# Kernel tuning notes

Hardware: AMD Instinct MI355X
Metric: run time of the kernel (lower is better)

The kernel has to match this reference:

```python
import jax, jax.numpy as jnp
import numpy as np
import math

B = 2048
N_IN, N_H, N_OUT = 1024, 1024, 512
MAX_STEPS = 2                 # number of Gibbs sweeps (original loops until max_steps)
TEMP_A, TEMP_B = 2.0, 5.0     # temp_coeffs: T(step) = A / exp(step / B)
N_UPD = N_H + N_OUT           # visible layer is clamped (x given, unlock_vis=False)


def setup_inputs() -> dict:
    key = jax.random.key(0)
    ks = jax.random.split(key, 9)
    # binary states, as produced by torch.bernoulli(0.5) in init_state
    x = jax.random.bernoulli(ks[0], 0.5, (B, N_IN)).astype(jnp.float32)
    s1_init = jax.random.bernoulli(ks[1], 0.5, (B, N_H)).astype(jnp.float32)
    s2_init = jax.random.bernoulli(ks[2], 0.5, (B, N_OUT)).astype(jnp.float32)
    W1 = jax.random.normal(ks[3], (N_H, N_IN), jnp.float32) * 0.02
    b1 = jax.random.normal(ks[4], (N_H,), jnp.float32) * 0.02
    W2 = jax.random.normal(ks[5], (N_OUT, N_H), jnp.float32) * 0.02
    b2 = jax.random.normal(ks[6], (N_OUT,), jnp.float32) * 0.02
    # one random permutation of the 1536 free units per sweep (torch.randperm)
    ids = jnp.concatenate([
        jax.random.permutation(jax.random.fold_in(ks[7], s), N_UPD)
        for s in range(MAX_STEPS)
    ]).astype(jnp.int32)                      # [MAX_STEPS * N_UPD]
    # uniforms for the Bernoulli draws (torch.rand per node update)
    u = jax.random.uniform(ks[8], (MAX_STEPS * N_UPD, B), jnp.float32)
    return dict(x=x, s1_init=s1_init, s2_init=s2_init,
                W1=W1, b1=b1, W2=W2, b2=b2, u=u, ids=ids)


def reference(x, s1_init, s2_init, W1, b1, W2, b2, u, ids):
    # per-update temperature: sweep s has T = TEMP_A / exp(s / TEMP_B)
    temps = jnp.repeat(
        jnp.array([TEMP_A / math.exp(s / TEMP_B) for s in range(MAX_STEPS)],
                  dtype=jnp.float32),
        N_UPD)                                # [MAX_STEPS * N_UPD]

    def step(carry, inp):
        s1, s2 = carry
        gid, uu, T = inp                      # gid: global unit id in [0, N_UPD)

        def upd_hidden(s1, s2):
            n = gid                           # hidden unit index
            # gap = state[0] @ W1[n,:] + b1[n] + state[2] @ W2[:,n]
            gap = x @ W1[n] + b1[n] + s2 @ W2[:, n]      # [B]
            act = (jax.nn.sigmoid(gap / T) > uu).astype(s1.dtype)
            return s1.at[:, n].set(act), s2

        def upd_output(s1, s2):
            n = gid - N_H                     # output unit index
            # gap = state[1] @ W2[n,:] + b2[n]  (top layer: no layer above)
            gap = s1 @ W2[n] + b2[n]                     # [B]
            act = (jax.nn.sigmoid(gap / T) > uu).astype(s2.dtype)
            return s1, s2.at[:, n].set(act)

        s1, s2 = jax.lax.cond(gid < N_H, upd_hidden, upd_output, s1, s2)
        return (s1, s2), None

    (s1, s2), _ = jax.lax.scan(step, (s1_init, s2_init), (ids, u, temps))
    # state = [x (clamped visible), hidden, output], returned concatenated
    return jnp.concatenate([x, s1, s2], axis=-1)      # [B, N_IN+N_H+N_OUT]
```

## Files before the change

### kernel.cpp

```cpp
#include <hip/hip_runtime.h>
#include <math.h>

#define B_TOT   2048
#define N_IN    1024
#define N_H     1024
#define N_OUT   512
#define N_UPD   1536
#define T_TOT   3072
#define N_WIN   48


__global__ void prep_w1t(const float* __restrict__ W1, float* __restrict__ W1T) {
    int idx = blockIdx.x * 256 + threadIdx.x;
    int r = idx & 1023;
    int c = idx >> 10;
    W1T[(size_t)c * 1024 + r] = W1[(size_t)r * 1024 + c];
}

__global__ void prep_w2tf(const float* __restrict__ W2, float* __restrict__ W2Tf) {
    int idx = blockIdx.x * 256 + threadIdx.x;
    int r = idx & 511;
    int c = idx >> 9;
    W2Tf[(size_t)c * 512 + r] = W2[(size_t)r * 1024 + c];
}

__global__ void prep_whf(const float* __restrict__ W2, float* __restrict__ WHf) {
    int idx = blockIdx.x * 256 + threadIdx.x;
    int n = idx >> 9;
    int r = idx & 511;
    int l = r >> 3, j = r & 7;
    WHf[idx] = W2[(size_t)(j * 64 + l) * 1024 + n];
}

__global__ void prep_wof(const float* __restrict__ W2, float* __restrict__ WOf) {
    int idx = blockIdx.x * 256 + threadIdx.x;
    int nn = idx >> 10;
    int r = idx & 1023;
    int l = r >> 4, j = r & 15;
    WOf[idx] = W2[(size_t)nn * 1024 + j * 64 + l];
}

__global__ void prep_wx(const float* __restrict__ W2, const int* __restrict__ ids,
                        float* __restrict__ WXf) {
    int idx = blockIdx.x * 256 + threadIdx.x;
    int w = idx >> 12;
    int j = (idx >> 6) & 63;
    int l = idx & 63;
    int mj = ids[w * 64 + j];
    int nl = ids[w * 64 + l];
    float v = 0.0f;
    if (mj < N_H && nl >= N_H) v = W2[(size_t)(nl - N_H) * 1024 + mj];
    else if (mj >= N_H && nl < N_H) v = W2[(size_t)(mj - N_H) * 1024 + nl];
    WXf[idx] = v;
}

__global__ void prep_pos(const int* __restrict__ ids, int* __restrict__ posA,
                         int* __restrict__ posB) {
    int t = blockIdx.x * 256 + threadIdx.x;
    int n = ids[t];
    if (t < N_UPD) posA[n] = t; else posB[n] = t - N_UPD;
}

__global__ void prep_pos2(const int* __restrict__ ids, const int* __restrict__ posA,
                          int* __restrict__ pos2) {
    int t = blockIdx.x * 256 + threadIdx.x;
    pos2[t] = posA[ids[N_UPD + t]];
}

__global__ __launch_bounds__(256) void prep_th(const float* __restrict__ u,
                                               double* __restrict__ thT) {
    __shared__ double tile[64][65];
    int bt = blockIdx.x % 48;
    int bb = blockIdx.x / 48;
    int tx = threadIdx.x & 63;
    int ty0 = threadIdx.x >> 6;
    const double T1c = (double)(float)(2.0 / exp((double)1 / 5.0));
    for (int r = ty0; r < 64; r += 4) {
        int t = bt * 64 + r;
        double ud = (double)u[(size_t)t * 2048 + bb * 64 + tx];
        double T = (t >= N_UPD) ? T1c : 2.0;
        tile[r][tx] = T * (log(ud) - log1p(-ud));
    }
    __syncthreads();
    for (int r = ty0; r < 64; r += 4)
        thT[(size_t)(bb * 64 + r) * 3072 + bt * 64 + tx] = tile[tx][r];
}

__global__ void copy_x(const float* __restrict__ x, float* __restrict__ out) {
    int idx = blockIdx.x * 256 + threadIdx.x;
    int b = idx >> 8, c = idx & 255;
    ((float4*)(out + (size_t)b * 2560))[c] = ((const float4*)(x + (size_t)b * 1024))[c];
}


#define FMA32(M, DW) { \
    a0  = fma(((M) & 0x00000001u) ? 1.0 : 0.0, (DW), a0 ); \
    a1  = fma(((M) & 0x00000002u) ? 1.0 : 0.0, (DW), a1 ); \
    a2  = fma(((M) & 0x00000004u) ? 1.0 : 0.0, (DW), a2 ); \
    a3  = fma(((M) & 0x00000008u) ? 1.0 : 0.0, (DW), a3 ); \
    a4  = fma(((M) & 0x00000010u) ? 1.0 : 0.0, (DW), a4 ); \
    a5  = fma(((M) & 0x00000020u) ? 1.0 : 0.0, (DW), a5 ); \
    a6  = fma(((M) & 0x00000040u) ? 1.0 : 0.0, (DW), a6 ); \
    a7  = fma(((M) & 0x00000080u) ? 1.0 : 0.0, (DW), a7 ); \
    a8  = fma(((M) & 0x00000100u) ? 1.0 : 0.0, (DW), a8 ); \
    a9  = fma(((M) & 0x00000200u) ? 1.0 : 0.0, (DW), a9 ); \
    a10 = fma(((M) & 0x00000400u) ? 1.0 : 0.0, (DW), a10); \
    a11 = fma(((M) & 0x00000800u) ? 1.0 : 0.0, (DW), a11); \
    a12 = fma(((M) & 0x00001000u) ? 1.0 : 0.0, (DW), a12); \
    a13 = fma(((M) & 0x00002000u) ? 1.0 : 0.0, (DW), a13); \
    a14 = fma(((M) & 0x00004000u) ? 1.0 : 0.0, (DW), a14); \
    a15 = fma(((M) & 0x00008000u) ? 1.0 : 0.0, (DW), a15); \
    a16 = fma(((M) & 0x00010000u) ? 1.0 : 0.0, (DW), a16); \
    a17 = fma(((M) & 0x00020000u) ? 1.0 : 0.0, (DW), a17); \
    a18 = fma(((M) & 0x00040000u) ? 1.0 : 0.0, (DW), a18); \
    a19 = fma(((M) & 0x00080000u) ? 1.0 : 0.0, (DW), a19); \
    a20 = fma(((M) & 0x00100000u) ? 1.0 : 0.0, (DW), a20); \
    a21 = fma(((M) & 0x00200000u) ? 1.0 : 0.0, (DW), a21); \
    a22 = fma(((M) & 0x00400000u) ? 1.0 : 0.0, (DW), a22); \
    a23 = fma(((M) & 0x00800000u) ? 1.0 : 0.0, (DW), a23); \
    a24 = fma(((M) & 0x01000000u) ? 1.0 : 0.0, (DW), a24); \
    a25 = fma(((M) & 0x02000000u) ? 1.0 : 0.0, (DW), a25); \
    a26 = fma(((M) & 0x04000000u) ? 1.0 : 0.0, (DW), a26); \
    a27 = fma(((M) & 0x08000000u) ? 1.0 : 0.0, (DW), a27); \
    a28 = fma(((M) & 0x10000000u) ? 1.0 : 0.0, (DW), a28); \
    a29 = fma(((M) & 0x20000000u) ? 1.0 : 0.0, (DW), a29); \
    a30 = fma(((M) & 0x40000000u) ? 1.0 : 0.0, (DW), a30); \
    a31 = fma(((M) & 0x80000000u) ? 1.0 : 0.0, (DW), a31); }

#define FMA16(M, DW) { \
    a0  = fma(((M) & 0x0001u) ? 1.0 : 0.0, (DW), a0 ); \
    a1  = fma(((M) & 0x0002u) ? 1.0 : 0.0, (DW), a1 ); \
    a2  = fma(((M) & 0x0004u) ? 1.0 : 0.0, (DW), a2 ); \
    a3  = fma(((M) & 0x0008u) ? 1.0 : 0.0, (DW), a3 ); \
    a4  = fma(((M) & 0x0010u) ? 1.0 : 0.0, (DW), a4 ); \
    a5  = fma(((M) & 0x0020u) ? 1.0 : 0.0, (DW), a5 ); \
    a6  = fma(((M) & 0x0040u) ? 1.0 : 0.0, (DW), a6 ); \
    a7  = fma(((M) & 0x0080u) ? 1.0 : 0.0, (DW), a7 ); \
    a8  = fma(((M) & 0x0100u) ? 1.0 : 0.0, (DW), a8 ); \
    a9  = fma(((M) & 0x0200u) ? 1.0 : 0.0, (DW), a9 ); \
    a10 = fma(((M) & 0x0400u) ? 1.0 : 0.0, (DW), a10); \
    a11 = fma(((M) & 0x0800u) ? 1.0 : 0.0, (DW), a11); \
    a12 = fma(((M) & 0x1000u) ? 1.0 : 0.0, (DW), a12); \
    a13 = fma(((M) & 0x2000u) ? 1.0 : 0.0, (DW), a13); \
    a14 = fma(((M) & 0x4000u) ? 1.0 : 0.0, (DW), a14); \
    a15 = fma(((M) & 0x8000u) ? 1.0 : 0.0, (DW), a15); }

__global__ __launch_bounds__(256) void init_h1(
    const float* __restrict__ x, const float* __restrict__ s2i,
    const float* __restrict__ W1T, const float* __restrict__ W2,
    const float* __restrict__ b1, double* __restrict__ h1g)
{
    const int tid = threadIdx.x;
    const int ug  = blockIdx.x & 3;
    const int b0  = (blockIdx.x >> 2) << 5;
    const int n   = (ug << 8) + tid;

    __shared__ unsigned xm[1024];
    __shared__ unsigned s2m[512];

    for (int i = tid; i < 1024; i += 256) {
        unsigned m = 0;
        #pragma unroll
        for (int bb = 0; bb < 32; ++bb)
            m |= (x[(size_t)(b0 + bb) * 1024 + i] != 0.0f) ? (1u << bb) : 0u;
        xm[i] = m;
    }
    for (int j = tid; j < 512; j += 256) {
        unsigned m = 0;
        #pragma unroll
        for (int bb = 0; bb < 32; ++bb)
            m |= (s2i[(size_t)(b0 + bb) * 512 + j] != 0.0f) ? (1u << bb) : 0u;
        s2m[j] = m;
    }
    __syncthreads();

    double a0, a1, a2, a3, a4, a5, a6, a7, a8, a9, a10, a11, a12, a13, a14, a15,
           a16, a17, a18, a19, a20, a21, a22, a23, a24, a25, a26, a27, a28, a29,
           a30, a31;
    {
        double bv = (double)b1[n];
        a0 = bv; a1 = bv; a2 = bv; a3 = bv; a4 = bv; a5 = bv; a6 = bv; a7 = bv;
        a8 = bv; a9 = bv; a10 = bv; a11 = bv; a12 = bv; a13 = bv; a14 = bv; a15 = bv;
        a16 = bv; a17 = bv; a18 = bv; a19 = bv; a20 = bv; a21 = bv; a22 = bv; a23 = bv;
        a24 = bv; a25 = bv; a26 = bv; a27 = bv; a28 = bv; a29 = bv; a30 = bv; a31 = bv;
    }

    {
        float wc0, wc1, wc2, wc3, wc4, wc5, wc6, wc7;
        {
            const float* q = W1T + n;
            wc0 = q[0];    wc1 = q[1024]; wc2 = q[2048]; wc3 = q[3072];
            wc4 = q[4096]; wc5 = q[5120]; wc6 = q[6144]; wc7 = q[7168];
        }
        for (int i0 = 0; i0 < 1024; i0 += 8) {
            float wn0, wn1, wn2, wn3, wn4, wn5, wn6, wn7;
            if (i0 + 8 < 1024) {
                const float* q = W1T + (size_t)(i0 + 8) * 1024 + n;
                wn0 = q[0];    wn1 = q[1024]; wn2 = q[2048]; wn3 = q[3072];
                wn4 = q[4096]; wn5 = q[5120]; wn6 = q[6144]; wn7 = q[7168];
            } else {
                wn0 = wc0; wn1 = wc1; wn2 = wc2; wn3 = wc3;
                wn4 = wc4; wn5 = wc5; wn6 = wc6; wn7 = wc7;
            }
            unsigned m0 = (unsigned)__builtin_amdgcn_readfirstlane((int)xm[i0 + 0]);
            unsigned m1 = (unsigned)__builtin_amdgcn_readfirstlane((int)xm[i0 + 1]);
            unsigned m2 = (unsigned)__builtin_amdgcn_readfirstlane((int)xm[i0 + 2]);
            unsigned m3 = (unsigned)__builtin_amdgcn_readfirstlane((int)xm[i0 + 3]);
            unsigned m4 = (unsigned)__builtin_amdgcn_readfirstlane((int)xm[i0 + 4]);
            unsigned m5 = (unsigned)__builtin_amdgcn_readfirstlane((int)xm[i0 + 5]);
            unsigned m6 = (unsigned)__builtin_amdgcn_readfirstlane((int)xm[i0 + 6]);
            unsigned m7 = (unsigned)__builtin_amdgcn_readfirstlane((int)xm[i0 + 7]);
            double dw;
            dw = (double)wc0; FMA32(m0, dw);
            dw = (double)wc1; FMA32(m1, dw);
            dw = (double)wc2; FMA32(m2, dw);
            dw = (double)wc3; FMA32(m3, dw);
            dw = (double)wc4; FMA32(m4, dw);
            dw = (double)wc5; FMA32(m5, dw);
            dw = (double)wc6; FMA32(m6, dw);
            dw = (double)wc7; FMA32(m7, dw);
            wc0 = wn0; wc1 = wn1; wc2 = wn2; wc3 = wn3;
            wc4 = wn4; wc5 = wn5; wc6 = wn6; wc7 = wn7;
        }
    }
    {
        float wc0, wc1, wc2, wc3, wc4, wc5, wc6, wc7;
        {
            const float* q = W2 + n;
            wc0 = q[0];    wc1 = q[1024]; wc2 = q[2048]; wc3 = q[3072];
            wc4 = q[4096]; wc5 = q[5120]; wc6 = q[6144]; wc7 = q[7168];
        }
        for (int i0 = 0; i0 < 512; i0 += 8) {
            float wn0, wn1, wn2, wn3, wn4, wn5, wn6, wn7;
            if (i0 + 8 < 512) {
                const float* q = W2 + (size_t)(i0 + 8) * 1024 + n;
                wn0 = q[0];    wn1 = q[1024]; wn2 = q[2048]; wn3 = q[3072];
                wn4 = q[4096]; wn5 = q[5120]; wn6 = q[6144]; wn7 = q[7168];
            } else {
                wn0 = wc0; wn1 = wc1; wn2 = wc2; wn3 = wc3;
                wn4 = wc4; wn5 = wc5; wn6 = wc6; wn7 = wc7;
            }
            unsigned m0 = (unsigned)__builtin_amdgcn_readfirstlane((int)s2m[i0 + 0]);
            unsigned m1 = (unsigned)__builtin_amdgcn_readfirstlane((int)s2m[i0 + 1]);
            unsigned m2 = (unsigned)__builtin_amdgcn_readfirstlane((int)s2m[i0 + 2]);
            unsigned m3 = (unsigned)__builtin_amdgcn_readfirstlane((int)s2m[i0 + 3]);
            unsigned m4 = (unsigned)__builtin_amdgcn_readfirstlane((int)s2m[i0 + 4]);
            unsigned m5 = (unsigned)__builtin_amdgcn_readfirstlane((int)s2m[i0 + 5]);
            unsigned m6 = (unsigned)__builtin_amdgcn_readfirstlane((int)s2m[i0 + 6]);
            unsigned m7 = (unsigned)__builtin_amdgcn_readfirstlane((int)s2m[i0 + 7]);
            double dw;
            dw = (double)wc0; FMA32(m0, dw);
            dw = (double)wc1; FMA32(m1, dw);
            dw = (double)wc2; FMA32(m2, dw);
            dw = (double)wc3; FMA32(m3, dw);
            dw = (double)wc4; FMA32(m4, dw);
            dw = (double)wc5; FMA32(m5, dw);
            dw = (double)wc6; FMA32(m6, dw);
            dw = (double)wc7; FMA32(m7, dw);
            wc0 = wn0; wc1 = wn1; wc2 = wn2; wc3 = wn3;
            wc4 = wn4; wc5 = wn5; wc6 = wn6; wc7 = wn7;
        }
    }

    h1g[(size_t)(b0 + 0)  * 1024 + n] = a0;
    h1g[(size_t)(b0 + 1)  * 1024 + n] = a1;
    h1g[(size_t)(b0 + 2)  * 1024 + n] = a2;
    h1g[(size_t)(b0 + 3)  * 1024 + n] = a3;
    h1g[(size_t)(b0 + 4)  * 1024 + n] = a4;
    h1g[(size_t)(b0 + 5)  * 1024 + n] = a5;
    h1g[(size_t)(b0 + 6)  * 1024 + n] = a6;
    h1g[(size_t)(b0 + 7)  * 1024 + n] = a7;
    h1g[(size_t)(b0 + 8)  * 1024 + n] = a8;
    h1g[(size_t)(b0 + 9)  * 1024 + n] = a9;
    h1g[(size_t)(b0 + 10) * 1024 + n] = a10;
    h1g[(size_t)(b0 + 11) * 1024 + n] = a11;
    h1g[(size_t)(b0 + 12) * 1024 + n] = a12;
    h1g[(size_t)(b0 + 13) * 1024 + n] = a13;
    h1g[(size_t)(b0 + 14) * 1024 + n] = a14;
    h1g[(size_t)(b0 + 15) * 1024 + n] = a15;
    h1g[(size_t)(b0 + 16) * 1024 + n] = a16;
    h1g[(size_t)(b0 + 17) * 1024 + n] = a17;
    h1g[(size_t)(b0 + 18) * 1024 + n] = a18;
    h1g[(size_t)(b0 + 19) * 1024 + n] = a19;
    h1g[(size_t)(b0 + 20) * 1024 + n] = a20;
    h1g[(size_t)(b0 + 21) * 1024 + n] = a21;
    h1g[(size_t)(b0 + 22) * 1024 + n] = a22;
    h1g[(size_t)(b0 + 23) * 1024 + n] = a23;
    h1g[(size_t)(b0 + 24) * 1024 + n] = a24;
    h1g[(size_t)(b0 + 25) * 1024 + n] = a25;
    h1g[(size_t)(b0 + 26) * 1024 + n] = a26;
    h1g[(size_t)(b0 + 27) * 1024 + n] = a27;
    h1g[(size_t)(b0 + 28) * 1024 + n] = a28;
    h1g[(size_t)(b0 + 29) * 1024 + n] = a29;
    h1g[(size_t)(b0 + 30) * 1024 + n] = a30;
    h1g[(size_t)(b0 + 31) * 1024 + n] = a31;
}

__global__ __launch_bounds__(256) void init_h2(
    const float* __restrict__ s1i, const float* __restrict__ W2Tf,
    const float* __restrict__ b2, double* __restrict__ h2g)
{
    const int tid = threadIdx.x;
    const int ug  = blockIdx.x & 1;
    const int b0  = (blockIdx.x >> 1) << 4;
    const int nn  = (ug << 8) + tid;

    __shared__ unsigned short s1m[1024];

    for (int i = tid; i < 1024; i += 256) {
        unsigned m = 0;
        #pragma unroll
        for (int bb = 0; bb < 16; ++bb)
            m |= (s1i[(size_t)(b0 + bb) * 1024 + i] != 0.0f) ? (1u << bb) : 0u;
        s1m[i] = (unsigned short)m;
    }
    __syncthreads();

    double a0, a1, a2, a3, a4, a5, a6, a7, a8, a9, a10, a11, a12, a13, a14, a15;
    {
        double bv = (double)b2[nn];
        a0 = bv; a1 = bv; a2 = bv; a3 = bv; a4 = bv; a5 = bv; a6 = bv; a7 = bv;
        a8 = bv; a9 = bv; a10 = bv; a11 = bv; a12 = bv; a13 = bv; a14 = bv; a15 = bv;
    }

    {
        float wc0, wc1, wc2, wc3, wc4, wc5, wc6, wc7;
        {
            const float* q = W2Tf + nn;
            wc0 = q[0];    wc1 = q[512];  wc2 = q[1024]; wc3 = q[1536];
            wc4 = q[2048]; wc5 = q[2560]; wc6 = q[3072]; wc7 = q[3584];
        }
        for (int i0 = 0; i0 < 1024; i0 += 8) {
            float wn0, wn1, wn2, wn3, wn4, wn5, wn6, wn7;
            if (i0 + 8 < 1024) {
                const float* q = W2Tf + (size_t)(i0 + 8) * 512 + nn;
                wn0 = q[0];    wn1 = q[512];  wn2 = q[1024]; wn3 = q[1536];
                wn4 = q[2048]; wn5 = q[2560]; wn6 = q[3072]; wn7 = q[3584];
            } else {
                wn0 = wc0; wn1 = wc1; wn2 = wc2; wn3 = wc3;
                wn4 = wc4; wn5 = wc5; wn6 = wc6; wn7 = wc7;
            }
            unsigned m0 = (unsigned)__builtin_amdgcn_readfirstlane((int)s1m[i0 + 0]);
            unsigned m1 = (unsigned)__builtin_amdgcn_readfirstlane((int)s1m[i0 + 1]);
            unsigned m2 = (unsigned)__builtin_amdgcn_readfirstlane((int)s1m[i0 + 2]);
            unsigned m3 = (unsigned)__builtin_amdgcn_readfirstlane((int)s1m[i0 + 3]);
            unsigned m4 = (unsigned)__builtin_amdgcn_readfirstlane((int)s1m[i0 + 4]);
            unsigned m5 = (unsigned)__builtin_amdgcn_readfirstlane((int)s1m[i0 + 5]);
            unsigned m6 = (unsigned)__builtin_amdgcn_readfirstlane((int)s1m[i0 + 6]);
            unsigned m7 = (unsigned)__builtin_amdgcn_readfirstlane((int)s1m[i0 + 7]);
            double dw;
            dw = (double)wc0; FMA16(m0, dw);
            dw = (double)wc1; FMA16(m1, dw);
            dw = (double)wc2; FMA16(m2, dw);
            dw = (double)wc3; FMA16(m3, dw);
            dw = (double)wc4; FMA16(m4, dw);
            dw = (double)wc5; FMA16(m5, dw);
            dw = (double)wc6; FMA16(m6, dw);
            dw = (double)wc7; FMA16(m7, dw);
            wc0 = wn0; wc1 = wn1; wc2 = wn2; wc3 = wn3;
            wc4 = wn4; wc5 = wn5; wc6 = wn6; wc7 = wn7;
        }
    }

    h2g[(size_t)(b0 + 0)  * 512 + nn] = a0;
    h2g[(size_t)(b0 + 1)  * 512 + nn] = a1;
    h2g[(size_t)(b0 + 2)  * 512 + nn] = a2;
    h2g[(size_t)(b0 + 3)  * 512 + nn] = a3;
    h2g[(size_t)(b0 + 4)  * 512 + nn] = a4;
    h2g[(size_t)(b0 + 5)  * 512 + nn] = a5;
    h2g[(size_t)(b0 + 6)  * 512 + nn] = a6;
    h2g[(size_t)(b0 + 7)  * 512 + nn] = a7;
    h2g[(size_t)(b0 + 8)  * 512 + nn] = a8;
    h2g[(size_t)(b0 + 9)  * 512 + nn] = a9;
    h2g[(size_t)(b0 + 10) * 512 + nn] = a10;
    h2g[(size_t)(b0 + 11) * 512 + nn] = a11;
    h2g[(size_t)(b0 + 12) * 512 + nn] = a12;
    h2g[(size_t)(b0 + 13) * 512 + nn] = a13;
    h2g[(size_t)(b0 + 14) * 512 + nn] = a14;
    h2g[(size_t)(b0 + 15) * 512 + nn] = a15;
}


#define LOADQ(NC, Q0, Q1, Q2, Q3) { \
    if ((NC) < N_H) { \
        const float4* p_ = (const float4*)(WHf + ((size_t)(NC) << 9) + (lane << 3)); \
        Q0 = p_[0]; Q1 = p_[1]; Q2 = Q1; Q3 = Q1; \
    } else { \
        const float4* p_ = (const float4*)(WOf + ((size_t)((NC) - N_H) << 10) + (lane << 4)); \
        Q0 = p_[0]; Q1 = p_[1]; Q2 = p_[2]; Q3 = p_[3]; \
    } }

#define APPLYQ(JC, NC, Q0, Q1, Q2, Q3) { \
    const double sd = ((A >> (JC)) & 1ull) ? 1.0 : -1.0; \
    if ((NC) < N_H) { \
        h2r[0] = fma(sd, (double)Q0.x, h2r[0]); \
        h2r[1] = fma(sd, (double)Q0.y, h2r[1]); \
        h2r[2] = fma(sd, (double)Q0.z, h2r[2]); \
        h2r[3] = fma(sd, (double)Q0.w, h2r[3]); \
        h2r[4] = fma(sd, (double)Q1.x, h2r[4]); \
        h2r[5] = fma(sd, (double)Q1.y, h2r[5]); \
        h2r[6] = fma(sd, (double)Q1.z, h2r[6]); \
        h2r[7] = fma(sd, (double)Q1.w, h2r[7]); \
    } else { \
        h1r[0]  = fma(sd, (double)Q0.x, h1r[0]); \
        h1r[1]  = fma(sd, (double)Q0.y, h1r[1]); \
        h1r[2]  = fma(sd, (double)Q0.z, h1r[2]); \
        h1r[3]  = fma(sd, (double)Q0.w, h1r[3]); \
        h1r[4]  = fma(sd, (double)Q1.x, h1r[4]); \
        h1r[5]  = fma(sd, (double)Q1.y, h1r[5]); \
        h1r[6]  = fma(sd, (double)Q1.z, h1r[6]); \
        h1r[7]  = fma(sd, (double)Q1.w, h1r[7]); \
        h1r[8]  = fma(sd, (double)Q2.x, h1r[8]); \
        h1r[9]  = fma(sd, (double)Q2.y, h1r[9]); \
        h1r[10] = fma(sd, (double)Q2.z, h1r[10]); \
        h1r[11] = fma(sd, (double)Q2.w, h1r[11]); \
        h1r[12] = fma(sd, (double)Q3.x, h1r[12]); \
        h1r[13] = fma(sd, (double)Q3.y, h1r[13]); \
        h1r[14] = fma(sd, (double)Q3.z, h1r[14]); \
        h1r[15] = fma(sd, (double)Q3.w, h1r[15]); \
    } }

#define DECLB(S) \
    int c##S = 0; \
    int j##S##0 = 0, j##S##1 = 0, j##S##2 = 0, j##S##3 = 0; \
    int n##S##0 = 0, n##S##1 = 0, n##S##2 = 0, n##S##3 = 0; \
    float4 S##q00, S##q01, S##q02, S##q03; \
    float4 S##q10, S##q11, S##q12, S##q13; \
    float4 S##q20, S##q21, S##q22, S##q23; \
    float4 S##q30, S##q31, S##q32, S##q33;

#define EXTRACTB(S) { \
    c##S = 0; \
    if (C) { \
        j##S##0 = __builtin_ctzll(C); C &= C - 1; \
        n##S##0 = __builtin_amdgcn_readlane(idw, j##S##0); \
        LOADQ(n##S##0, S##q00, S##q01, S##q02, S##q03); c##S = 1; \
        if (C) { \
            j##S##1 = __builtin_ctzll(C); C &= C - 1; \
            n##S##1 = __builtin_amdgcn_readlane(idw, j##S##1); \
            LOADQ(n##S##1, S##q10, S##q11, S##q12, S##q13); c##S = 2; \
            if (C) { \
                j##S##2 = __builtin_ctzll(C); C &= C - 1; \
                n##S##2 = __builtin_amdgcn_readlane(idw, j##S##2); \
                LOADQ(n##S##2, S##q20, S##q21, S##q22, S##q23); c##S = 3; \
                if (C) { \
                    j##S##3 = __builtin_ctzll(C); C &= C - 1; \
                    n##S##3 = __builtin_amdgcn_readlane(idw, j##S##3); \
                    LOADQ(n##S##3, S##q30, S##q31, S##q32, S##q33); c##S = 4; \
                } } } } }

#define APPLYB(S) { \
    APPLYQ(j##S##0, n##S##0, S##q00, S##q01, S##q02, S##q03); \
    if (c##S > 1) APPLYQ(j##S##1, n##S##1, S##q10, S##q11, S##q12, S##q13); \
    if (c##S > 2) APPLYQ(j##S##2, n##S##2, S##q20, S##q21, S##q22, S##q23); \
    if (c##S > 3) APPLYQ(j##S##3, n##S##3, S##q30, S##q31, S##q32, S##q33); }

__global__ __launch_bounds__(64, 2) void gibbs(
    const double* __restrict__ thT, const int* __restrict__ ids,
    const float* __restrict__ WHf, const float* __restrict__ WOf,
    const float* __restrict__ WXf,
    const int* __restrict__ pos2, const int* __restrict__ posB,
    const double* __restrict__ h1g, const double* __restrict__ h2g,
    const float* __restrict__ s1i, const float* __restrict__ s2i,
    float* __restrict__ out)
{
    const int lane = threadIdx.x;
    const int b = blockIdx.x;

    __shared__ double fld[1536];
    __shared__ unsigned long long act[N_WIN];
    __shared__ unsigned long long sb[24];

    double h1r[16], h2r[8];
    #pragma unroll
    for (int k = 0; k < 16; ++k)
        h1r[k] = __builtin_nontemporal_load(&h1g[(size_t)b * 1024 + k * 64 + lane]);
    #pragma unroll
    for (int k = 0; k < 8; ++k)
        h2r[k] = __builtin_nontemporal_load(&h2g[(size_t)b * 512 + k * 64 + lane]);

    #pragma unroll
    for (int k = 0; k < 16; ++k) {
        float v = __builtin_nontemporal_load(&s1i[(size_t)b * 1024 + k * 64 + lane]);
        unsigned long long m = __ballot(v != 0.0f);
        if (lane == 0) sb[k] = m;
    }
    #pragma unroll
    for (int k = 0; k < 8; ++k) {
        float v = __builtin_nontemporal_load(&s2i[(size_t)b * 512 + k * 64 + lane]);
        unsigned long long m = __ballot(v != 0.0f);
        if (lane == 0) sb[16 + k] = m;
    }

    int idw = ids[lane];
    double thc = __builtin_nontemporal_load(&thT[(size_t)b * 3072 + lane]);
    int p2c = 0;

    for (int w = 0; w < N_WIN; ++w) {
        const int t0 = w * 64;

        const float* wxp = WXf + ((size_t)w << 12) + lane;
        float wx32[64];
        #pragma unroll
        for (int j = 0; j < 64; ++j) wx32[j] = wxp[(size_t)j * 64];

        int idn = 0; double thn = 0.0; int p2n = 0;
        if (w + 1 < N_WIN) {
            idn = ids[t0 + 64 + lane];
            thn = __builtin_nontemporal_load(&thT[(size_t)b * 3072 + t0 + 64 + lane]);
            if (w + 1 >= 24) p2n = pos2[(w + 1 - 24) * 64 + lane];
        }

        int oldb;
        if (w < 24) {
            unsigned long long sv = sb[idw >> 6];
            oldb = (int)((sv >> (idw & 63)) & 1ull);
        } else {
            unsigned long long av = act[p2c >> 6];
            oldb = (int)((av >> (p2c & 63)) & 1ull);
        }
        unsigned long long OLD = __ballot(oldb != 0);

        #pragma unroll
        for (int k = 0; k < 16; ++k) fld[k * 64 + lane] = h1r[k];
        #pragma unroll
        for (int k = 0; k < 8; ++k)  fld[1024 + k * 64 + lane] = h2r[k];
        double g = fld[idw];

        unsigned long long A = 0;
        #pragma unroll
        for (int j = 0; j < 64; ++j) {
            unsigned long long bal = __ballot(g > thc);
            unsigned long long aj = (bal >> j) & 1ull;
            A |= aj << j;
            unsigned long long o = (OLD >> j) & 1ull;
            unsigned long long du = aj ? (o ? 0ull : 0x3FF0000000000000ull)
                                       : (o ? 0xBFF0000000000000ull : 0ull);
            g = fma(__builtin_bit_cast(double, du), (double)wx32[j], g);
        }
        if (lane == 0) act[w] = A;

        if (w + 1 < N_WIN) {
            unsigned long long C = A ^ OLD;
            if (C) {
                DECLB(a)
                DECLB(b)
                EXTRACTB(a)
                for (;;) {
                    EXTRACTB(b)
                    APPLYB(a)
                    if (cb == 0) break;
                    EXTRACTB(a)
                    APPLYB(b)
                    if (ca == 0) break;
                }
            }
        }

        idw = idn; thc = thn; p2c = p2n;
    }

    #pragma unroll
    for (int k = 0; k < 16; ++k) {
        int p = posB[k * 64 + lane];
        unsigned long long av = act[24 + (p >> 6)];
        __builtin_nontemporal_store((float)((av >> (p & 63)) & 1ull),
                                    &out[(size_t)b * 2560 + 1024 + k * 64 + lane]);
    }
    #pragma unroll
    for (int k = 0; k < 8; ++k) {
        int p = posB[1024 + k * 64 + lane];
        unsigned long long av = act[24 + (p >> 6)];
        __builtin_nontemporal_store((float)((av >> (p & 63)) & 1ull),
                                    &out[(size_t)b * 2560 + 2048 + k * 64 + lane]);
    }
}

extern "C" void kernel_launch(void* const* d_in, const int* in_sizes, int n_in,
                              void* d_out, int out_size, void* d_ws, size_t ws_size,
                              hipStream_t stream) {
    const float* x   = (const float*)d_in[0];
    const float* s1i = (const float*)d_in[1];
    const float* s2i = (const float*)d_in[2];
    const float* W1  = (const float*)d_in[3];
    const float* b1  = (const float*)d_in[4];
    const float* W2  = (const float*)d_in[5];
    const float* b2  = (const float*)d_in[6];
    const float* u   = (const float*)d_in[7];
    const int*   ids = (const int*)d_in[8];
    float* out = (float*)d_out;

    char* ws = (char*)d_ws;
    float*  W1T  = (float*) (ws);
    float*  W2Tf = (float*) (ws + ((size_t)4  << 20));
    float*  WHf  = (float*) (ws + ((size_t)6  << 20));
    float*  WOf  = (float*) (ws + ((size_t)8  << 20));
    float*  WXf  = (float*) (ws + ((size_t)10 << 20));
    int*    posA = (int*)   (ws + ((size_t)11 << 20));
    int*    posB = (int*)   (ws + ((size_t)11 << 20) + 8192);
    int*    pos2 = (int*)   (ws + ((size_t)11 << 20) + 16384);
    double* thT  = (double*)(ws + ((size_t)12 << 20));
    double* h1g  = (double*)(ws + ((size_t)60 << 20));
    double* h2g  = (double*)(ws + ((size_t)76 << 20));

    hipLaunchKernelGGL(prep_w1t,  dim3(4096), dim3(256), 0, stream, W1, W1T);
    hipLaunchKernelGGL(prep_w2tf, dim3(2048), dim3(256), 0, stream, W2, W2Tf);
    hipLaunchKernelGGL(prep_whf,  dim3(2048), dim3(256), 0, stream, W2, WHf);
    hipLaunchKernelGGL(prep_wof,  dim3(2048), dim3(256), 0, stream, W2, WOf);
    hipLaunchKernelGGL(prep_wx,   dim3(768),  dim3(256), 0, stream, W2, ids, WXf);
    hipLaunchKernelGGL(prep_pos,  dim3(12),   dim3(256), 0, stream, ids, posA, posB);
    hipLaunchKernelGGL(prep_pos2, dim3(6),    dim3(256), 0, stream, ids, posA, pos2);
    hipLaunchKernelGGL(prep_th,   dim3(1536), dim3(256), 0, stream, u, thT);
    hipLaunchKernelGGL(copy_x,    dim3(2048), dim3(256), 0, stream, x, out);
    hipLaunchKernelGGL(init_h1,   dim3(256),  dim3(256), 0, stream,
                       x, s2i, W1T, W2, b1, h1g);
    hipLaunchKernelGGL(init_h2,   dim3(256),  dim3(256), 0, stream,
                       s1i, W2Tf, b2, h2g);
    hipLaunchKernelGGL(gibbs, dim3(2048), dim3(64), 0, stream,
                       thT, ids, WHf, WOf, WXf, pos2, posB, h1g, h2g, s1i, s2i, out);
}
```

Measured before the change: 1.249 ms.

## Process two batch rows per wavefront, sharing weight loads across both

```diff
diff --git a/kernel.cpp b/kernel.cpp
--- a/kernel.cpp
+++ b/kernel.cpp
@@ -390,70 +390,39 @@
         Q0 = p_[0]; Q1 = p_[1]; Q2 = p_[2]; Q3 = p_[3]; \
     } }
 
-#define APPLYQ(JC, NC, Q0, Q1, Q2, Q3) { \
-    const double sd = ((A >> (JC)) & 1ull) ? 1.0 : -1.0; \
+#define APPLYF(H1, H2, AV, JC, NC, Q0, Q1, Q2, Q3) { \
+    const double sd = (((AV) >> (JC)) & 1ull) ? 1.0 : -1.0; \
     if ((NC) < N_H) { \
-        h2r[0] = fma(sd, (double)Q0.x, h2r[0]); \
-        h2r[1] = fma(sd, (double)Q0.y, h2r[1]); \
-        h2r[2] = fma(sd, (double)Q0.z, h2r[2]); \
-        h2r[3] = fma(sd, (double)Q0.w, h2r[3]); \
-        h2r[4] = fma(sd, (double)Q1.x, h2r[4]); \
-        h2r[5] = fma(sd, (double)Q1.y, h2r[5]); \
-        h2r[6] = fma(sd, (double)Q1.z, h2r[6]); \
-        h2r[7] = fma(sd, (double)Q1.w, h2r[7]); \
+        H2[0] = fma(sd, (double)Q0.x, H2[0]); \
+        H2[1] = fma(sd, (double)Q0.y, H2[1]); \
+        H2[2] = fma(sd, (double)Q0.z, H2[2]); \
+        H2[3] = fma(sd, (double)Q0.w, H2[3]); \
+        H2[4] = fma(sd, (double)Q1.x, H2[4]); \
+        H2[5] = fma(sd, (double)Q1.y, H2[5]); \
+        H2[6] = fma(sd, (double)Q1.z, H2[6]); \
+        H2[7] = fma(sd, (double)Q1.w, H2[7]); \
     } else { \
-        h1r[0]  = fma(sd, (double)Q0.x, h1r[0]); \
-        h1r[1]  = fma(sd, (double)Q0.y, h1r[1]); \
-        h1r[2]  = fma(sd, (double)Q0.z, h1r[2]); \
-        h1r[3]  = fma(sd, (double)Q0.w, h1r[3]); \
-        h1r[4]  = fma(sd, (double)Q1.x, h1r[4]); \
-        h1r[5]  = fma(sd, (double)Q1.y, h1r[5]); \
-        h1r[6]  = fma(sd, (double)Q1.z, h1r[6]); \
-        h1r[7]  = fma(sd, (double)Q1.w, h1r[7]); \
-        h1r[8]  = fma(sd, (double)Q2.x, h1r[8]); \
-        h1r[9]  = fma(sd, (double)Q2.y, h1r[9]); \
-        h1r[10] = fma(sd, (double)Q2.z, h1r[10]); \
-        h1r[11] = fma(sd, (double)Q2.w, h1r[11]); \
-        h1r[12] = fma(sd, (double)Q3.x, h1r[12]); \
-        h1r[13] = fma(sd, (double)Q3.y, h1r[13]); \
-        h1r[14] = fma(sd, (double)Q3.z, h1r[14]); \
-        h1r[15] = fma(sd, (double)Q3.w, h1r[15]); \
+        H1[0]  = fma(sd, (double)Q0.x, H1[0]); \
+        H1[1]  = fma(sd, (double)Q0.y, H1[1]); \
+        H1[2]  = fma(sd, (double)Q0.z, H1[2]); \
+        H1[3]  = fma(sd, (double)Q0.w, H1[3]); \
+        H1[4]  = fma(sd, (double)Q1.x, H1[4]); \
+        H1[5]  = fma(sd, (double)Q1.y, H1[5]); \
+        H1[6]  = fma(sd, (double)Q1.z, H1[6]); \
+        H1[7]  = fma(sd, (double)Q1.w, H1[7]); \
+        H1[8]  = fma(sd, (double)Q2.x, H1[8]); \
+        H1[9]  = fma(sd, (double)Q2.y, H1[9]); \
+        H1[10] = fma(sd, (double)Q2.z, H1[10]); \
+        H1[11] = fma(sd, (double)Q2.w, H1[11]); \
+        H1[12] = fma(sd, (double)Q3.x, H1[12]); \
+        H1[13] = fma(sd, (double)Q3.y, H1[13]); \
+        H1[14] = fma(sd, (double)Q3.z, H1[14]); \
+        H1[15] = fma(sd, (double)Q3.w, H1[15]); \
     } }
 
-#define DECLB(S) \
-    int c##S = 0; \
-    int j##S##0 = 0, j##S##1 = 0, j##S##2 = 0, j##S##3 = 0; \
-    int n##S##0 = 0, n##S##1 = 0, n##S##2 = 0, n##S##3 = 0; \
-    float4 S##q00, S##q01, S##q02, S##q03; \
-    float4 S##q10, S##q11, S##q12, S##q13; \
-    float4 S##q20, S##q21, S##q22, S##q23; \
-    float4 S##q30, S##q31, S##q32, S##q33;
-
-#define EXTRACTB(S) { \
-    c##S = 0; \
-    if (C) { \
-        j##S##0 = __builtin_ctzll(C); C &= C - 1; \
-        n##S##0 = __builtin_amdgcn_readlane(idw, j##S##0); \
-        LOADQ(n##S##0, S##q00, S##q01, S##q02, S##q03); c##S = 1; \
-        if (C) { \
-            j##S##1 = __builtin_ctzll(C); C &= C - 1; \
-            n##S##1 = __builtin_amdgcn_readlane(idw, j##S##1); \
-            LOADQ(n##S##1, S##q10, S##q11, S##q12, S##q13); c##S = 2; \
-            if (C) { \
-                j##S##2 = __builtin_ctzll(C); C &= C - 1; \
-                n##S##2 = __builtin_amdgcn_readlane(idw, j##S##2); \
-                LOADQ(n##S##2, S##q20, S##q21, S##q22, S##q23); c##S = 3; \
-                if (C) { \
-                    j##S##3 = __builtin_ctzll(C); C &= C - 1; \
-                    n##S##3 = __builtin_amdgcn_readlane(idw, j##S##3); \
-                    LOADQ(n##S##3, S##q30, S##q31, S##q32, S##q33); c##S = 4; \
-                } } } } }
-
-#define APPLYB(S) { \
-    APPLYQ(j##S##0, n##S##0, S##q00, S##q01, S##q02, S##q03); \
-    if (c##S > 1) APPLYQ(j##S##1, n##S##1, S##q10, S##q11, S##q12, S##q13); \
-    if (c##S > 2) APPLYQ(j##S##2, n##S##2, S##q20, S##q21, S##q22, S##q23); \
-    if (c##S > 3) APPLYQ(j##S##3, n##S##3, S##q30, S##q31, S##q32, S##q33); }
+#define APPLY2(J, N, Q0, Q1, Q2, Q3) { \
+    if ((CA >> (J)) & 1ull) APPLYF(h1A, h2A, AA, J, N, Q0, Q1, Q2, Q3); \
+    if ((CB >> (J)) & 1ull) APPLYF(h1B, h2B, AB, J, N, Q0, Q1, Q2, Q3); }
 
 __global__ __launch_bounds__(64, 2) void gibbs(
     const double* __restrict__ thT, const int* __restrict__ ids,
@@ -465,35 +434,45 @@
     float* __restrict__ out)
 {
     const int lane = threadIdx.x;
-    const int b = blockIdx.x;
-
-    __shared__ double fld[1536];
-    __shared__ unsigned long long act[N_WIN];
-    __shared__ unsigned long long sb[24];
-
-    double h1r[16], h2r[8];
-    #pragma unroll
-    for (int k = 0; k < 16; ++k)
-        h1r[k] = __builtin_nontemporal_load(&h1g[(size_t)b * 1024 + k * 64 + lane]);
-    #pragma unroll
-    for (int k = 0; k < 8; ++k)
-        h2r[k] = __builtin_nontemporal_load(&h2g[(size_t)b * 512 + k * 64 + lane]);
-
+    const int bA = blockIdx.x * 2;
+    const int bB = bA + 1;
+
+    __shared__ double fldA[1536], fldB[1536];
+    __shared__ unsigned long long actA[N_WIN], actB[N_WIN];
+    __shared__ unsigned long long sbA[24], sbB[24];
+
+    double h1A[16], h2A[8], h1B[16], h2B[8];
     #pragma unroll
     for (int k = 0; k < 16; ++k) {
-        float v = __builtin_nontemporal_load(&s1i[(size_t)b * 1024 + k * 64 + lane]);
-        unsigned long long m = __ballot(v != 0.0f);
-        if (lane == 0) sb[k] = m;
+        h1A[k] = __builtin_nontemporal_load(&h1g[(size_t)bA * 1024 + k * 64 + lane]);
+        h1B[k] = __builtin_nontemporal_load(&h1g[(size_t)bB * 1024 + k * 64 + lane]);
     }
     #pragma unroll
     for (int k = 0; k < 8; ++k) {
-        float v = __builtin_nontemporal_load(&s2i[(size_t)b * 512 + k * 64 + lane]);
-        unsigned long long m = __ballot(v != 0.0f);
-        if (lane == 0) sb[16 + k] = m;
+        h2A[k] = __builtin_nontemporal_load(&h2g[(size_t)bA * 512 + k * 64 + lane]);
+        h2B[k] = __builtin_nontemporal_load(&h2g[(size_t)bB * 512 + k * 64 + lane]);
+    }
+
+    #pragma unroll
+    for (int k = 0; k < 16; ++k) {
+        float vA = __builtin_nontemporal_load(&s1i[(size_t)bA * 1024 + k * 64 + lane]);
+        float vB = __builtin_nontemporal_load(&s1i[(size_t)bB * 1024 + k * 64 + lane]);
+        unsigned long long mA = __ballot(vA != 0.0f);
+        unsigned long long mB = __ballot(vB != 0.0f);
+        if (lane == 0) { sbA[k] = mA; sbB[k] = mB; }
+    }
+    #pragma unroll
+    for (int k = 0; k < 8; ++k) {
+        float vA = __builtin_nontemporal_load(&s2i[(size_t)bA * 512 + k * 64 + lane]);
+        float vB = __builtin_nontemporal_load(&s2i[(size_t)bB * 512 + k * 64 + lane]);
+        unsigned long long mA = __ballot(vA != 0.0f);
+        unsigned long long mB = __ballot(vB != 0.0f);
+        if (lane == 0) { sbA[16 + k] = mA; sbB[16 + k] = mB; }
     }
 
     int idw = ids[lane];
-    double thc = __builtin_nontemporal_load(&thT[(size_t)b * 3072 + lane]);
+    double thcA = __builtin_nontemporal_load(&thT[(size_t)bA * 3072 + lane]);
+    double thcB = __builtin_nontemporal_load(&thT[(size_t)bB * 3072 + lane]);
     int p2c = 0;
 
     for (int w = 0; w < N_WIN; ++w) {
@@ -504,75 +483,113 @@
         #pragma unroll
         for (int j = 0; j < 64; ++j) wx32[j] = wxp[(size_t)j * 64];
 
-        int idn = 0; double thn = 0.0; int p2n = 0;
+        int idn = 0; double thnA = 0.0, thnB = 0.0; int p2n = 0;
         if (w + 1 < N_WIN) {
             idn = ids[t0 + 64 + lane];
-            thn = __builtin_nontemporal_load(&thT[(size_t)b * 3072 + t0 + 64 + lane]);
+            thnA = __builtin_nontemporal_load(&thT[(size_t)bA * 3072 + t0 + 64 + lane]);
+            thnB = __builtin_nontemporal_load(&thT[(size_t)bB * 3072 + t0 + 64 + lane]);
             if (w + 1 >= 24) p2n = pos2[(w + 1 - 24) * 64 + lane];
         }
 
-        int oldb;
+        int oldA, oldB;
         if (w < 24) {
-            unsigned long long sv = sb[idw >> 6];
-            oldb = (int)((sv >> (idw & 63)) & 1ull);
+            unsigned long long svA = sbA[idw >> 6];
+            unsigned long long svB = sbB[idw >> 6];
+            oldA = (int)((svA >> (idw & 63)) & 1ull);
+            oldB = (int)((svB >> (idw & 63)) & 1ull);
         } else {
-            unsigned long long av = act[p2c >> 6];
-            oldb = (int)((av >> (p2c & 63)) & 1ull);
-        }
-        unsigned long long OLD = __ballot(oldb != 0);
+            unsigned long long avA = actA[p2c >> 6];
+            unsigned long long avB = actB[p2c >> 6];
+            oldA = (int)((avA >> (p2c & 63)) & 1ull);
+            oldB = (int)((avB >> (p2c & 63)) & 1ull);
+        }
+        unsigned long long OLDA = __ballot(oldA != 0);
+        unsigned long long OLDB = __ballot(oldB != 0);
 
         #pragma unroll
-        for (int k = 0; k < 16; ++k) fld[k * 64 + lane] = h1r[k];
+        for (int k = 0; k < 16; ++k) { fldA[k * 64 + lane] = h1A[k]; fldB[k * 64 + lane] = h1B[k]; }
         #pragma unroll
-        for (int k = 0; k < 8; ++k)  fld[1024 + k * 64 + lane] = h2r[k];
-        double g = fld[idw];
-
-        unsigned long long A = 0;
+        for (int k = 0; k < 8; ++k)  { fldA[1024 + k * 64 + lane] = h2A[k]; fldB[1024 + k * 64 + lane] = h2B[k]; }
+        double gA = fldA[idw];
+        double gB = fldB[idw];
+
+        unsigned long long AA = 0, AB = 0;
         #pragma unroll
         for (int j = 0; j < 64; ++j) {
-            unsigned long long bal = __ballot(g > thc);
-            unsigned long long aj = (bal >> j) & 1ull;
-            A |= aj << j;
-            unsigned long long o = (OLD >> j) & 1ull;
-            unsigned long long du = aj ? (o ? 0ull : 0x3FF0000000000000ull)
-                                       : (o ? 0xBFF0000000000000ull : 0ull);
-            g = fma(__builtin_bit_cast(double, du), (double)wx32[j], g);
-        }
-        if (lane == 0) act[w] = A;
+            unsigned long long balA = __ballot(gA > thcA);
+            unsigned long long balB = __ballot(gB > thcB);
+            unsigned long long aA = (balA >> j) & 1ull;
+            unsigned long long aB = (balB >> j) & 1ull;
+            AA |= aA << j;
+            AB |= aB << j;
+            unsigned long long oA = (OLDA >> j) & 1ull;
+            unsigned long long oB = (OLDB >> j) & 1ull;
+            unsigned long long duA = aA ? (oA ? 0ull : 0x3FF0000000000000ull)
+                                        : (oA ? 0xBFF0000000000000ull : 0ull);
+            unsigned long long duB = aB ? (oB ? 0ull : 0x3FF0000000000000ull)
+                                        : (oB ? 0xBFF0000000000000ull : 0ull);
+            double wd = (double)wx32[j];
+            gA = fma(__builtin_bit_cast(double, duA), wd, gA);
+            gB = fma(__builtin_bit_cast(double, duB), wd, gB);
+        }
+        if (lane == 0) { actA[w] = AA; actB[w] = AB; }
 
         if (w + 1 < N_WIN) {
-            unsigned long long C = A ^ OLD;
-            if (C) {
-                DECLB(a)
-                DECLB(b)
-                EXTRACTB(a)
-                for (;;) {
-                    EXTRACTB(b)
-                    APPLYB(a)
-                    if (cb == 0) break;
-                    EXTRACTB(a)
-                    APPLYB(b)
-                    if (ca == 0) break;
+            unsigned long long CA = AA ^ OLDA;
+            unsigned long long CB = AB ^ OLDB;
+            unsigned long long CU = CA | CB;
+            while (CU) {
+                int j0 = __builtin_ctzll(CU); CU &= CU - 1;
+                int n0 = __builtin_amdgcn_readlane(idw, j0);
+                int j1 = 0, n1 = 0, j2 = 0, n2 = 0, j3 = 0, n3 = 0;
+                int cnt = 1;
+                if (CU) {
+                    j1 = __builtin_ctzll(CU); CU &= CU - 1;
+                    n1 = __builtin_amdgcn_readlane(idw, j1); cnt = 2;
+                    if (CU) {
+                        j2 = __builtin_ctzll(CU); CU &= CU - 1;
+                        n2 = __builtin_amdgcn_readlane(idw, j2); cnt = 3;
+                        if (CU) {
+                            j3 = __builtin_ctzll(CU); CU &= CU - 1;
+                            n3 = __builtin_amdgcn_readlane(idw, j3); cnt = 4;
+                        }
+                    }
                 }
+                float4 a0, a1, a2, a3, b0, b1, b2, b3;
+                float4 c0, c1, c2, c3, d0, d1, d2, d3;
+                LOADQ(n0, a0, a1, a2, a3);
+                if (cnt > 1) LOADQ(n1, b0, b1, b2, b3);
+                if (cnt > 2) LOADQ(n2, c0, c1, c2, c3);
+                if (cnt > 3) LOADQ(n3, d0, d1, d2, d3);
+                APPLY2(j0, n0, a0, a1, a2, a3);
+                if (cnt > 1) APPLY2(j1, n1, b0, b1, b2, b3);
+                if (cnt > 2) APPLY2(j2, n2, c0, c1, c2, c3);
+                if (cnt > 3) APPLY2(j3, n3, d0, d1, d2, d3);
             }
         }
 
-        idw = idn; thc = thn; p2c = p2n;
+        idw = idn; thcA = thnA; thcB = thnB; p2c = p2n;
     }
 
     #pragma unroll
     for (int k = 0; k < 16; ++k) {
         int p = posB[k * 64 + lane];
-        unsigned long long av = act[24 + (p >> 6)];
-        __builtin_nontemporal_store((float)((av >> (p & 63)) & 1ull),
-                                    &out[(size_t)b * 2560 + 1024 + k * 64 + lane]);
+        unsigned long long avA = actA[24 + (p >> 6)];
+        unsigned long long avB = actB[24 + (p >> 6)];
+        __builtin_nontemporal_store((float)((avA >> (p & 63)) & 1ull),
+                                    &out[(size_t)bA * 2560 + 1024 + k * 64 + lane]);
+        __builtin_nontemporal_store((float)((avB >> (p & 63)) & 1ull),
+                                    &out[(size_t)bB * 2560 + 1024 + k * 64 + lane]);
     }
     #pragma unroll
     for (int k = 0; k < 8; ++k) {
         int p = posB[1024 + k * 64 + lane];
-        unsigned long long av = act[24 + (p >> 6)];
-        __builtin_nontemporal_store((float)((av >> (p & 63)) & 1ull),
-                                    &out[(size_t)b * 2560 + 2048 + k * 64 + lane]);
+        unsigned long long avA = actA[24 + (p >> 6)];
+        unsigned long long avB = actB[24 + (p >> 6)];
+        __builtin_nontemporal_store((float)((avA >> (p & 63)) & 1ull),
+                                    &out[(size_t)bA * 2560 + 2048 + k * 64 + lane]);
+        __builtin_nontemporal_store((float)((avB >> (p & 63)) & 1ull),
+                                    &out[(size_t)bB * 2560 + 2048 + k * 64 + lane]);
     }
 }
 
@@ -616,6 +633,6 @@
                        x, s2i, W1T, W2, b1, h1g);
     hipLaunchKernelGGL(init_h2,   dim3(256),  dim3(256), 0, stream,
                        s1i, W2Tf, b2, h2g);
-    hipLaunchKernelGGL(gibbs, dim3(2048), dim3(64), 0, stream,
+    hipLaunchKernelGGL(gibbs, dim3(1024), dim3(64), 0, stream,
                        thT, ids, WHf, WOf, WXf, pos2, posB, h1g, h2g, s1i, s2i, out);
 }
```

Result: slower. 1.772 ms (+41.8%).
